# Performance work log

Hardware: AMD Instinct MI355X
Metric: run time of the kernel (lower is better)

Reference implementation:

```python
import jax, jax.numpy as jnp
import numpy as np

DIM = 1024
SEQ_LEN = 4096
K = 256
HEADS = 16
DIM_HEAD = DIM // HEADS  # 64
BATCH = 4


def setup_inputs() -> dict:
    key = jax.random.key(0)
    ks = jax.random.split(key, 8)
    x = jax.random.normal(ks[0], (BATCH, SEQ_LEN, DIM), dtype=jnp.float32)
    # nn.Linear weights are [out, in]; y = x @ W.T
    std_lin = 1.0 / np.sqrt(DIM)
    Wq = jax.random.uniform(ks[1], (HEADS * DIM_HEAD, DIM), minval=-std_lin, maxval=std_lin, dtype=jnp.float32)
    Wk = jax.random.uniform(ks[2], (HEADS * DIM_HEAD, DIM), minval=-std_lin, maxval=std_lin, dtype=jnp.float32)
    Wv = jax.random.uniform(ks[3], (HEADS * DIM_HEAD, DIM), minval=-std_lin, maxval=std_lin, dtype=jnp.float32)
    # proj_k/proj_v init_: uniform(-1/sqrt(k), 1/sqrt(k)) on [seq_len, k]
    std_p = 1.0 / np.sqrt(K)
    proj_k = jax.random.uniform(ks[4], (SEQ_LEN, K), minval=-std_p, maxval=std_p, dtype=jnp.float32)
    proj_v = jax.random.uniform(ks[5], (SEQ_LEN, K), minval=-std_p, maxval=std_p, dtype=jnp.float32)
    std_o = 1.0 / np.sqrt(HEADS * DIM_HEAD)
    Wo = jax.random.uniform(ks[6], (DIM, HEADS * DIM_HEAD), minval=-std_o, maxval=std_o, dtype=jnp.float32)
    bo = jax.random.uniform(ks[7], (DIM,), minval=-std_o, maxval=std_o, dtype=jnp.float32)
    return {"x": x, "Wq": Wq, "Wk": Wk, "Wv": Wv, "proj_k": proj_k, "proj_v": proj_v, "Wo": Wo, "bo": bo}


def reference(x, Wq, Wk, Wv, proj_k, proj_v, Wo, bo):
    b, n, d = x.shape
    h, dh, k = HEADS, DIM_HEAD, K
    # q/k/v projections
    q = jnp.einsum('bnd,ed->bne', x, Wq)            # [b, n, h*dh]
    keys = jnp.einsum('bnd,ed->bne', x, Wk)         # [b, n, h*dh]
    vals = jnp.einsum('bnd,ed->bne', x, Wv)         # [b, n, h*dh]
    # low-rank projection along sequence: [b, n, e] x [n, k] -> [b, k, e]
    keys = jnp.einsum('bne,nk->bke', keys, proj_k[:n])
    vals = jnp.einsum('bne,nk->bke', vals, proj_v[:n])
    # split heads
    q = q.reshape(b, n, h, dh).transpose(0, 2, 1, 3)        # [b, h, n, dh]
    keys = keys.reshape(b, k, h, dh).transpose(0, 2, 1, 3)  # [b, h, k, dh]
    vals = vals.reshape(b, k, h, dh).transpose(0, 2, 1, 3)  # [b, h, k, dh]
    dots = jnp.einsum('bhnd,bhkd->bhnk', q, keys) * (dh ** -0.5)
    attn = jax.nn.softmax(dots, axis=-1)
    out = jnp.einsum('bhnk,bhkd->bhnd', attn, vals)
    out = out.transpose(0, 2, 1, 3).reshape(b, n, h * dh)
    return jnp.einsum('bne,oe->bno', out, Wo) + bo
```

## Files before the change

### kernel.cpp

```cpp
#include <hip/hip_runtime.h>
#include <hip/hip_bf16.h>
#include <stdint.h>

typedef unsigned short u16;
typedef __attribute__((ext_vector_type(8))) short bf16x8;
typedef __attribute__((ext_vector_type(4))) float f32x4;

#define DEV __device__ __forceinline__

DEV u16 f2bf(float f) {
  union { float f; unsigned u; } v; v.f = f;
  unsigned r = (v.u + 0x7fffu + ((v.u >> 16) & 1u)) >> 16;
  return (u16)r;
}

DEV unsigned pk2(float lo, float hi) {
  union { __hip_bfloat162 h; unsigned u; } c;
  c.h = __float22bfloat162_rn(make_float2(lo, hi));
  return c.u;
}

DEV f32x4 mfma16(bf16x8 a, bf16x8 b, f32x4 c) {
  return __builtin_amdgcn_mfma_f32_16x16x32_bf16(a, b, c, 0, 0, 0);
}

DEV void gload_lds16(const u16* g, u16* l) {
  __builtin_amdgcn_global_load_lds((const __attribute__((address_space(1))) void*)g,
                                   (__attribute__((address_space(3))) void*)l, 16, 0, 0);
}

#define QSCALE 0.18033688011112042f

__global__ void cvt_xpose_kernel(const float* __restrict__ src, u16* __restrict__ dst_rm,
                                 u16* __restrict__ dst_tp, int R, int C,
                                 long zS, long zRM, long zTP) {
  __shared__ u16 tile[64][72];
  src += (size_t)blockIdx.z * zS;
  dst_tp += (size_t)blockIdx.z * zTP;
  int r0 = blockIdx.y * 64, c0 = blockIdx.x * 64;
  int tr = threadIdx.x >> 2, tc = (threadIdx.x & 3) * 16;
  const float* s = src + (size_t)(r0 + tr) * C + c0 + tc;
  u16 loc[16];
#pragma unroll
  for (int q = 0; q < 4; ++q) {
    float4 v = ((const float4*)s)[q];
    loc[q * 4 + 0] = f2bf(v.x); loc[q * 4 + 1] = f2bf(v.y);
    loc[q * 4 + 2] = f2bf(v.z); loc[q * 4 + 3] = f2bf(v.w);
  }
#pragma unroll
  for (int i = 0; i < 16; ++i) tile[tr][tc + i] = loc[i];
  if (dst_rm) {
    u16* d = dst_rm + (size_t)blockIdx.z * zRM + (size_t)(r0 + tr) * C + c0 + tc;
    *(bf16x8*)d = *(const bf16x8*)&loc[0];
    *(bf16x8*)(d + 8) = *(const bf16x8*)&loc[8];
  }
  __syncthreads();
  u16 tmp[16];
#pragma unroll
  for (int i = 0; i < 16; ++i) tmp[i] = tile[tc + i][tr];
  u16* d = dst_tp + (size_t)(c0 + tr) * R + r0 + tc;
  *(bf16x8*)d = *(const bf16x8*)&tmp[0];
  *(bf16x8*)(d + 8) = *(const bf16x8*)&tmp[8];
}

__global__ void cvt_w4_kernel(const float* __restrict__ s0, const float* __restrict__ s1,
                              const float* __restrict__ s2, const float* __restrict__ s3,
                              u16* __restrict__ d0, u16* __restrict__ d1,
                              u16* __restrict__ d2, u16* __restrict__ d3) {
  const float* s; u16* d;
  switch (blockIdx.y) {
    case 0: s = s0; d = d0; break;
    case 1: s = s1; d = d1; break;
    case 2: s = s2; d = d2; break;
    default: s = s3; d = d3; break;
  }
  int i = blockIdx.x * 256 + threadIdx.x;
  float4 v = ((const float4*)s)[i];
  ushort4 o; o.x = f2bf(v.x); o.y = f2bf(v.y); o.z = f2bf(v.z); o.w = f2bf(v.w);
  ((ushort4*)d)[i] = o;
}

__global__ void reduce4_kernel(const float* __restrict__ part, u16* __restrict__ out) {
  int i = blockIdx.x * 256 + threadIdx.x;
  const float4* p = (const float4*)part;
  float4 a = p[i], b = p[i + 524288], c = p[i + 1048576], d = p[i + 1572864];
  ushort4 o;
  o.x = f2bf(a.x + b.x + c.x + d.x);
  o.y = f2bf(a.y + b.y + c.y + d.y);
  o.z = f2bf(a.z + b.z + c.z + d.z);
  o.w = f2bf(a.w + b.w + c.w + d.w);
  ((ushort4*)out)[i] = o;
}

template<int OMODE>
__global__ __launch_bounds__(256, 4)
void gemm_bt_kernel(const u16* __restrict__ A, const u16* __restrict__ Bt,
                    const u16* __restrict__ Bt2, void* __restrict__ Cout,
                    u16* __restrict__ CoutT, const float* __restrict__ bias, float cscale,
                    int ldA, int ldB, int ldC, int Klen,
                    long zA, long zB, long zC, int bMod, long kChunkA, long kChunkB) {
  __shared__ __align__(16) u16 smA[2][128 * 32];
  __shared__ __align__(16) u16 smB[2][128 * 32];
  const int t = threadIdx.x;
  const int lane = t & 63, wave = t >> 6;
  const int wm = wave & 1, wn = wave >> 1;
  const int g = lane >> 4, r = lane & 15;
  const int id = blockIdx.y * gridDim.x + blockIdx.x;
  const int cpx = (gridDim.x * gridDim.y) >> 3;
  const int s = (id & 7) * cpx + (id >> 3);
  const int bx = s % gridDim.x, by = s / gridDim.x;
  const int z = blockIdx.z;
  const int b = z % bMod, kc = z / bMod;
  const u16* Ab = A + (size_t)b * zA + (size_t)kc * kChunkA;
  const u16* Bbase = (Bt2 && (b & 1)) ? Bt2 : Bt;
  const u16* Bb = Bbase + (size_t)b * zB + (size_t)kc * kChunkB;
  const int m0 = by * 128, n0 = bx * 128;
  const int srow = t >> 2;
  const int lslot = ((t & 3) + 4 - ((srow >> 1) & 3)) & 3;

  f32x4 acc[4][4];
#pragma unroll
  for (int m = 0; m < 4; ++m)
#pragma unroll
    for (int n = 0; n < 4; ++n) acc[m][n] = f32x4{0.f, 0.f, 0.f, 0.f};

  auto STAGE = [&](int buf, int k0) {
#pragma unroll
    for (int p = 0; p < 2; ++p) {
      int row = p * 64 + srow;
      gload_lds16(Ab + (size_t)(m0 + row) * ldA + k0 + lslot * 8, &smA[buf][p * 2048 + wave * 512]);
      gload_lds16(Bb + (size_t)(n0 + row) * ldB + k0 + lslot * 8, &smB[buf][p * 2048 + wave * 512]);
    }
  };

  const int nt = Klen >> 5;
  STAGE(0, 0);
  __syncthreads();
  int cur = 0;
  for (int it = 0; it < nt; ++it) {
    if (it + 1 < nt) STAGE(cur ^ 1, (it + 1) << 5);
    bf16x8 af[4], bfr[4];
#pragma unroll
    for (int m = 0; m < 4; ++m) {
      int row = wm * 64 + m * 16 + r;
      int ps = (g + (row >> 1)) & 3;
      af[m] = *(const bf16x8*)&smA[cur][row * 32 + ps * 8];
    }
#pragma unroll
    for (int n = 0; n < 4; ++n) {
      int row = wn * 64 + n * 16 + r;
      int ps = (g + (row >> 1)) & 3;
      bfr[n] = *(const bf16x8*)&smB[cur][row * 32 + ps * 8];
    }
#pragma unroll
    for (int m = 0; m < 4; ++m)
#pragma unroll
      for (int n = 0; n < 4; ++n)
        acc[m][n] = mfma16(af[m], bfr[n], acc[m][n]);
    __syncthreads();
    cur ^= 1;
  }

  if constexpr (OMODE == 0) {
    u16* C = (u16*)Cout + (size_t)z * zC;
#pragma unroll
    for (int n = 0; n < 4; ++n) {
      int col = n0 + wn * 64 + n * 16 + r;
#pragma unroll
      for (int m = 0; m < 4; ++m) {
        int rowb = m0 + wm * 64 + m * 16 + 4 * g;
#pragma unroll
        for (int rr = 0; rr < 4; ++rr)
          C[(size_t)(rowb + rr) * ldC + col] = f2bf(acc[m][n][rr] * cscale);
      }
    }
  } else if constexpr (OMODE == 2) {
    float* myF = ((float*)(wave < 2 ? (void*)&smA[0][0] : (void*)&smB[0][0])) + (wave & 1) * 2048;
    float* Cg = (float*)Cout + (size_t)z * zC + (size_t)(m0 + wm * 64) * ldC + n0 + wn * 64;
#pragma unroll
    for (int np = 0; np < 2; ++np) {
#pragma unroll
      for (int n2 = 0; n2 < 2; ++n2)
#pragma unroll
        for (int m = 0; m < 4; ++m)
#pragma unroll
          for (int rr = 0; rr < 4; ++rr) {
            int rl = m * 16 + 4 * g + rr;
            int cl = n2 * 16 + r;
            myF[rl * 32 + ((((cl >> 2) ^ (rl & 7)) & 7) << 2) + (cl & 3)] =
                acc[m][np * 2 + n2][rr];
          }
      __syncthreads();
#pragma unroll
      for (int i = 0; i < 8; ++i) {
        int idx = i * 64 + lane;
        int row = idx >> 3, c = idx & 7;
        float4 v = *(const float4*)&myF[row * 32 + (((c ^ (row & 7)) & 7) << 2)];
        *(float4*)&Cg[(size_t)row * ldC + np * 32 + c * 4] = v;
      }
      __syncthreads();
    }
  } else if constexpr (OMODE == 3) {
    if ((z & 1) == 0) {
      u16* C = (u16*)Cout + (size_t)(z >> 1) * zC;
#pragma unroll
      for (int n = 0; n < 4; ++n) {
        int col = n0 + wn * 64 + n * 16 + r;
#pragma unroll
        for (int m = 0; m < 4; ++m) {
          int rowb = m0 + wm * 64 + m * 16 + 4 * g;
#pragma unroll
          for (int rr = 0; rr < 4; ++rr)
            C[(size_t)(rowb + rr) * ldC + col] = f2bf(acc[m][n][rr]);
        }
      }
    } else {
      u16* C = CoutT + (size_t)(z >> 1) * zC;
#pragma unroll
      for (int n = 0; n < 4; ++n) {
        int col = n0 + wn * 64 + n * 16 + r;
#pragma unroll
        for (int m = 0; m < 4; ++m) {
          int rowb = m0 + wm * 64 + m * 16 + 4 * g;
          ushort4 o;
          o.x = f2bf(acc[m][n][0]); o.y = f2bf(acc[m][n][1]);
          o.z = f2bf(acc[m][n][2]); o.w = f2bf(acc[m][n][3]);
          *(ushort4*)&C[(size_t)col * 256 + rowb] = o;
        }
      }
    }
  } else {
    float* C = (float*)Cout + (size_t)z * zC;
#pragma unroll
    for (int n = 0; n < 4; ++n) {
      int col = n0 + wn * 64 + n * 16 + r;
      float bv = (OMODE == 1) ? bias[col] : 0.f;
#pragma unroll
      for (int m = 0; m < 4; ++m) {
        int rowb = m0 + wm * 64 + m * 16 + 4 * g;
#pragma unroll
        for (int rr = 0; rr < 4; ++rr)
          C[(size_t)(rowb + rr) * ldC + col] = acc[m][n][rr] + bv;
      }
    }
  }
}

__global__ __launch_bounds__(512, 4)
void qgemm128_kernel(const u16* __restrict__ A, const u16* __restrict__ Bt,
                     u16* __restrict__ Cout, float cscale,
                     int ldA, int ldB, int ldC, int Klen) {
  __shared__ __align__(16) u16 lds[24576];
  const int t = threadIdx.x;
  const int lane = t & 63, wave = t >> 6;
  const int g = lane >> 4, r = lane & 15;
  const int wm = wave >> 2, wn = wave & 3;
  const int id = blockIdx.y * gridDim.x + blockIdx.x;
  const int cpx = (gridDim.x * gridDim.y) >> 3;
  const int s = (id & 7) * cpx + (id >> 3);
  const int bx = s & 3, by = s >> 2;
  const int m0 = by * 128, n0 = bx * 256;

  const int srow = t >> 2;
  const int lslot = ((t & 3) + 4 - ((srow >> 1) & 3)) & 3;

  auto STAGE = [&](int buf, int k0) {
    gload_lds16(A + (size_t)(m0 + srow) * ldA + k0 + lslot * 8,
                lds + buf * 4096 + t * 8);
#pragma unroll
    for (int p = 0; p < 2; ++p)
      gload_lds16(Bt + (size_t)(n0 + p * 128 + srow) * ldB + k0 + lslot * 8,
                  lds + 8192 + buf * 8192 + p * 4096 + t * 8);
  };

  f32x4 acc[4][4];
#pragma unroll
  for (int m = 0; m < 4; ++m)
#pragma unroll
    for (int n = 0; n < 4; ++n) acc[m][n] = f32x4{0.f, 0.f, 0.f, 0.f};

  const int nt = Klen >> 5;
  STAGE(0, 0);
  __syncthreads();
  int cur = 0;
  for (int it = 0; it < nt; ++it) {
    if (it + 1 < nt) STAGE(cur ^ 1, (it + 1) << 5);
    const u16* Ab = lds + cur * 4096;
    const u16* Bb = lds + 8192 + cur * 8192;
    bf16x8 af[4], bfr[4];
#pragma unroll
    for (int m = 0; m < 4; ++m) {
      int row = wm * 64 + m * 16 + r;
      int ps = (g + (row >> 1)) & 3;
      af[m] = *(const bf16x8*)&Ab[row * 32 + ps * 8];
    }
#pragma unroll
    for (int n = 0; n < 4; ++n) {
      int row = wn * 64 + n * 16 + r;
      int ps = (g + (row >> 1)) & 3;
      bfr[n] = *(const bf16x8*)&Bb[row * 32 + ps * 8];
    }
    __builtin_amdgcn_s_setprio(1);
#pragma unroll
    for (int m = 0; m < 4; ++m)
#pragma unroll
      for (int n = 0; n < 4; ++n)
        acc[m][n] = mfma16(af[m], bfr[n], acc[m][n]);
    __builtin_amdgcn_s_setprio(0);
    __syncthreads();
    cur ^= 1;
  }

  u16* myT = lds + wave * 2048;
  u16* Cg = Cout + (size_t)(m0 + wm * 64) * ldC + n0 + wn * 64;
#pragma unroll
  for (int np = 0; np < 2; ++np) {
#pragma unroll
    for (int n2 = 0; n2 < 2; ++n2)
#pragma unroll
      for (int m = 0; m < 4; ++m)
#pragma unroll
        for (int rr = 0; rr < 4; ++rr) {
          int rl = m * 16 + 4 * g + rr;
          int cl = n2 * 16 + r;
          myT[rl * 32 + (((cl >> 3) ^ (rl & 3)) << 3) + (cl & 7)] =
              f2bf(acc[m][np * 2 + n2][rr] * cscale);
        }
#pragma unroll
    for (int i = 0; i < 4; ++i) {
      int idx = i * 64 + lane;
      int row = idx >> 2, c = idx & 3;
      bf16x8 v = *(const bf16x8*)&myT[row * 32 + ((c ^ (row & 3)) << 3)];
      *(bf16x8*)&Cg[(size_t)row * ldC + np * 32 + c * 8] = v;
    }
  }
}

#define MFMA_CLUSTER(MH, NH, AF, BV)                                                    \
  do {                                                                                  \
    __builtin_amdgcn_s_setprio(1);                                                      \
    _Pragma("unroll")                                                                   \
    for (int mi = 0; mi < 4; ++mi)                                                      \
      _Pragma("unroll")                                                                 \
      for (int ni = 0; ni < 2; ++ni) {                                                  \
        acc[(MH)*4+mi][(NH)*2+ni] = mfma16(AF[mi][0], BV[ni][0], acc[(MH)*4+mi][(NH)*2+ni]); \
        acc[(MH)*4+mi][(NH)*2+ni] = mfma16(AF[mi][1], BV[ni][1], acc[(MH)*4+mi][(NH)*2+ni]); \
      }                                                                                 \
    __builtin_amdgcn_s_setprio(0);                                                      \
  } while (0)

#define ENDBAR(W)                                                                       \
  do {                                                                                  \
    if ((W) == 1) asm volatile("s_waitcnt vmcnt(4)" ::: "memory");                      \
    if ((W) == 2) asm volatile("s_waitcnt vmcnt(0)" ::: "memory");                      \
    __builtin_amdgcn_s_barrier();                                                       \
  } while (0)

template<int OMODE>
__global__ __launch_bounds__(512, 1)
void gemm256_kernel(const u16* __restrict__ A, const u16* __restrict__ Bt,
                    void* __restrict__ Cout, const float* __restrict__ bias,
                    float cscale, int ldA, int ldB, int ldC, int Klen) {
  __shared__ __align__(16) u16 lds[65536];
  const int t = threadIdx.x;
  const int lane = t & 63, wave = t >> 6;
  const int g = lane >> 4, r = lane & 15, rm = r & 7;
  const int wm = wave >> 2, wn = wave & 3;
  const int id = blockIdx.y * 4 + blockIdx.x;
  const int sw = (id & 7) * 32 + (id >> 3);
  const int bx = sw & 3, by = sw >> 2;
  const int m0 = by * 256, n0 = bx * 256;

  const int trow = t >> 3, tslot = t & 7;
  const int sslot = tslot ^ (trow & 7);
  const u16* Asrc = A + (size_t)(m0 + trow) * ldA + sslot * 8;
  const u16* Bsrc = Bt + sslot * 8;
  const int bRow0 = n0 + (trow >> 5) * 64 + (trow & 31);
  const int bRow1 = n0 + (2 + (trow >> 5)) * 64 + (trow & 31);

  u16* const A0 = lds;
  u16* const A1 = lds + 16384;
  u16* const B0 = lds + 32768;
  u16* const B1 = lds + 49152;

  auto stageA = [&](u16* buf, int h, int k0) {
    u16* d = buf + h * 8192 + t * 8;
    const u16* s0 = Asrc + (size_t)(h * 64) * ldA + k0;
    gload_lds16(s0, d);
    gload_lds16(s0 + (size_t)128 * ldA, d + 4096);
  };
  auto stageB = [&](u16* buf, int h, int k0) {
    u16* d = buf + h * 8192 + t * 8;
    gload_lds16(Bsrc + (size_t)(bRow0 + h * 32) * ldB + k0, d);
    gload_lds16(Bsrc + (size_t)(bRow1 + h * 32) * ldB + k0, d + 4096);
  };

  const int aoff = wm * 64 + r;
  const int boff = wn * 32 + r;

  auto loadA = [&](bf16x8 af[4][2], const u16* base, int MH) {
#pragma unroll
    for (int mi = 0; mi < 4; ++mi) {
      const u16* rp = base + (MH * 128 + aoff + mi * 16) * 64;
      af[mi][0] = *(const bf16x8*)&rp[(g ^ rm) * 8];
      af[mi][1] = *(const bf16x8*)&rp[((4 + g) ^ rm) * 8];
    }
  };
  auto loadB = [&](bf16x8 bv[2][2], const u16* base, int NH) {
#pragma unroll
    for (int ni = 0; ni < 2; ++ni) {
      const u16* rp = base + (NH * 128 + boff + ni * 16) * 64;
      bv[ni][0] = *(const bf16x8*)&rp[(g ^ rm) * 8];
      bv[ni][1] = *(const bf16x8*)&rp[((4 + g) ^ rm) * 8];
    }
  };

  f32x4 acc[8][4];
#pragma unroll
  for (int m = 0; m < 8; ++m)
#pragma unroll
    for (int n = 0; n < 4; ++n) acc[m][n] = f32x4{0.f, 0.f, 0.f, 0.f};

  stageA(A0, 0, 0); stageB(B0, 0, 0); stageA(A0, 1, 0); stageB(B0, 1, 0);
  stageA(A1, 0, 64); stageB(B1, 0, 64);
  asm volatile("s_waitcnt vmcnt(4)" ::: "memory");
  __builtin_amdgcn_s_barrier();

  const int nt = Klen >> 6;
  for (int j = 0; j < (nt >> 1); ++j) {
    const int ta = 2 * j, tb = ta + 1;
    const int more = (ta + 2 < nt);
    const int kb = tb * 64, kn = (ta + 2) * 64, kn2 = (tb + 2) * 64;
    bf16x8 af[4][2], bv0[2][2], bv1[2][2];
    loadA(af, A0, 0); loadB(bv0, B0, 0);
    stageA(A1, 1, kb);
    MFMA_CLUSTER(0, 0, af, bv0); ENDBAR(0);
    loadB(bv1, B0, 1);
    stageB(B1, 1, kb);
    MFMA_CLUSTER(0, 1, af, bv1); ENDBAR(0);
    loadA(af, A0, 1);
    if (more) stageA(A0, 0, kn);
    MFMA_CLUSTER(1, 0, af, bv0); ENDBAR(0);
    if (more) stageB(B0, 0, kn);
    MFMA_CLUSTER(1, 1, af, bv1); ENDBAR(more ? 1 : 2);
    loadA(af, A1, 0); loadB(bv0, B1, 0);
    if (more) stageA(A0, 1, kn);
    MFMA_CLUSTER(0, 0, af, bv0); ENDBAR(0);
    loadB(bv1, B1, 1);
    if (more) stageB(B0, 1, kn);
    MFMA_CLUSTER(0, 1, af, bv1); ENDBAR(0);
    loadA(af, A1, 1);
    if (more) stageA(A1, 0, kn2);
    MFMA_CLUSTER(1, 0, af, bv0); ENDBAR(0);
    if (more) stageB(B1, 0, kn2);
    MFMA_CLUSTER(1, 1, af, bv1); ENDBAR(more ? 1 : 2);
  }

  if constexpr (OMODE == 0) {
    u16* myT = lds + wave * 8192;
#pragma unroll
    for (int m = 0; m < 8; ++m)
#pragma unroll
      for (int n = 0; n < 4; ++n)
#pragma unroll
        for (int rr = 0; rr < 4; ++rr) {
          int rl = m * 16 + 4 * g + rr;
          int cl = n * 16 + r;
          myT[rl * 64 + (((cl >> 3) ^ (rl & 7)) << 3) + (cl & 7)] = f2bf(acc[m][n][rr] * cscale);
        }
    u16* Cg = (u16*)Cout + (size_t)(m0 + wm * 128) * ldC + n0 + wn * 64;
#pragma unroll
    for (int i = 0; i < 16; ++i) {
      int idx = i * 64 + lane;
      int row = idx >> 3, c8 = idx & 7;
      bf16x8 v = *(const bf16x8*)&myT[row * 64 + ((c8 ^ (row & 7)) << 3)];
      *(bf16x8*)&Cg[(size_t)row * ldC + c8 * 8] = v;
    }
  } else {
    float* myF = (float*)lds + wave * 4096;
    float bvn[4];
#pragma unroll
    for (int n = 0; n < 4; ++n) bvn[n] = bias[n0 + wn * 64 + n * 16 + r];
    float* Cg = (float*)Cout + (size_t)(m0 + wm * 128) * ldC + n0 + wn * 64;
#pragma unroll
    for (int half = 0; half < 2; ++half) {
#pragma unroll
      for (int m2 = 0; m2 < 4; ++m2)
#pragma unroll
        for (int n = 0; n < 4; ++n)
#pragma unroll
          for (int rr = 0; rr < 4; ++rr) {
            int rl = m2 * 16 + 4 * g + rr;
            int cl = n * 16 + r;
            myF[rl * 64 + (((cl >> 2) ^ (rl & 15)) << 2) + (cl & 3)] =
                acc[half * 4 + m2][n][rr] + bvn[n];
          }
#pragma unroll
      for (int i = 0; i < 16; ++i) {
        int idx = i * 64 + lane;
        int row = idx >> 4, c4 = idx & 15;
        float4 v = *(const float4*)&myF[row * 64 + ((c4 ^ (row & 15)) << 2)];
        *(float4*)&Cg[(size_t)(half * 64 + row) * ldC + c4 * 4] = v;
      }
    }
  }
}

__global__ __launch_bounds__(256, 3)
void attn_kernel(const u16* __restrict__ Q, const u16* __restrict__ Kl,
                 const u16* __restrict__ VT, u16* __restrict__ Out) {
  __shared__ __align__(16) u16 sm[24576];
  const int t = threadIdx.x, lane = t & 63, w = t >> 6;
  const int g = lane >> 4, r = lane & 15;
  const int id = (blockIdx.y << 6) | blockIdx.x;
  const int s = (id & 7) * (gridDim.y << 3) + (id >> 3);
  const int b = blockIdx.z, h = s >> 6, n0 = (s & 63) * 64;
  const u16* Kb = Kl + (size_t)b * 262144 + h * 64;
  const u16* Vb = VT + (size_t)b * 262144 + (size_t)(h * 64) * 256;
  u16* vbase = sm + 16384;

  const int vd = t >> 2;
  const int vsl = (t & 3) ^ (vd & 3);
  auto stage_slice = [&](int kk) {
    gload_lds16(Vb + (size_t)vd * 256 + kk * 32 + vsl * 8,
                vbase + (kk & 3) * 2048 + w * 512);
  };

#pragma unroll
  for (int p = 0; p < 8; ++p) {
    int row = p * 32 + (t >> 3);
    int ls = ((t & 7) + 8 - (row & 7)) & 7;
    gload_lds16(Kb + (size_t)row * 1024 + ls * 8, sm + p * 2048 + w * 512);
  }
#pragma unroll
  for (int kk = 0; kk < 4; ++kk) stage_slice(kk);
  const int qrow = n0 + w * 16 + r;
  const u16* Qp = Q + ((size_t)(b * 4096 + qrow)) * 1024 + h * 64 + g * 8;
  bf16x8 aq0 = *(const bf16x8*)Qp;
  bf16x8 aq1 = *(const bf16x8*)(Qp + 32);
  asm volatile("s_waitcnt vmcnt(4)" ::: "memory");
  __builtin_amdgcn_s_barrier();

  f32x4 dotv[16];
  __builtin_amdgcn_s_setprio(1);
#pragma unroll
  for (int kf = 0; kf < 16; ++kf) {
    int row = kf * 16 + r;
    bf16x8 kb0 = *(const bf16x8*)&sm[row * 64 + ((g + row) & 7) * 8];
    bf16x8 kb1 = *(const bf16x8*)&sm[row * 64 + ((4 + g + row) & 7) * 8];
    f32x4 d = f32x4{0.f, 0.f, 0.f, 0.f};
    d = mfma16(kb0, aq0, d);
    d = mfma16(kb1, aq1, d);
    dotv[kf] = d;
  }
  __builtin_amdgcn_s_setprio(0);
  asm volatile("s_waitcnt vmcnt(3)" ::: "memory");
  __builtin_amdgcn_s_barrier();

  float mx = -3.4e38f;
#pragma unroll
  for (int kf = 0; kf < 16; ++kf)
    mx = fmaxf(mx, fmaxf(fmaxf(dotv[kf][0], dotv[kf][1]), fmaxf(dotv[kf][2], dotv[kf][3])));
  mx = fmaxf(mx, __shfl_xor(mx, 16, 64));
  mx = fmaxf(mx, __shfl_xor(mx, 32, 64));
  float ssum = 0.f;
#pragma unroll
  for (int kf = 0; kf < 16; ++kf)
#pragma unroll
    for (int j = 0; j < 4; ++j) {
      float p = __builtin_amdgcn_exp2f(dotv[kf][j] - mx);
      dotv[kf][j] = p;
      ssum += p;
    }
  ssum += __shfl_xor(ssum, 16, 64);
  ssum += __shfl_xor(ssum, 32, 64);
  const float inv = 1.f / ssum;
  float invv[4];
#pragma unroll
  for (int rr = 0; rr < 4; ++rr) invv[rr] = __shfl(inv, 4 * g + rr, 64);

  const int q16 = w * 16 + r;
  const int qx = (q16 & 7) << 3;
#pragma unroll
  for (int kf = 0; kf < 16; ++kf) {
    uint2 val;
    val.x = pk2(dotv[kf][0], dotv[kf][1]);
    val.y = pk2(dotv[kf][2], dotv[kf][3]);
    *(uint2*)&sm[(q16 * 256 + kf * 16 + 4 * g) ^ qx] = val;
  }

  f32x4 oacc[4];
#pragma unroll
  for (int df = 0; df < 4; ++df) oacc[df] = f32x4{0.f, 0.f, 0.f, 0.f};
#pragma unroll
  for (int kk = 0; kk < 8; ++kk) {
    bf16x8 ap = *(const bf16x8*)&sm[(q16 * 256 + kk * 32 + g * 8) ^ qx];
    const u16* vb = vbase + (kk & 3) * 2048;
    __builtin_amdgcn_s_setprio(1);
#pragma unroll
    for (int df = 0; df < 4; ++df) {
      int d = df * 16 + r;
      bf16x8 bv = *(const bf16x8*)&vb[d * 32 + (g ^ (d & 3)) * 8];
      oacc[df] = mfma16(ap, bv, oacc[df]);
    }
    __builtin_amdgcn_s_setprio(0);
    if (kk < 7) {
      if (kk < 5)       asm volatile("s_waitcnt vmcnt(2)" ::: "memory");
      else if (kk == 5) asm volatile("s_waitcnt vmcnt(1)" ::: "memory");
      else              asm volatile("s_waitcnt vmcnt(0)" ::: "memory");
      __builtin_amdgcn_s_barrier();
      if (kk < 4) stage_slice(kk + 4);
    }
  }

  u16* myO = sm + w * 4096;
#pragma unroll
  for (int df = 0; df < 4; ++df)
#pragma unroll
    for (int rr = 0; rr < 4; ++rr) {
      int row = 4 * g + rr;
      int col = df * 16 + r;
      myO[row * 64 + (((col >> 3) ^ (row & 7)) << 3) + (col & 7)] = f2bf(oacc[df][rr] * invv[rr]);
    }
#pragma unroll
  for (int i = 0; i < 2; ++i) {
    int idx = i * 64 + lane;
    int row = idx >> 3, c8 = idx & 7;
    bf16x8 v = *(const bf16x8*)&myO[row * 64 + ((c8 ^ (row & 7)) << 3)];
    *(bf16x8*)&Out[((size_t)(b * 4096 + n0 + w * 16 + row)) * 1024 + h * 64 + c8 * 8] = v;
  }
}

extern "C" void kernel_launch(void* const* d_in, const int* in_sizes, int n_in,
                              void* d_out, int out_size, void* d_ws, size_t ws_size,
                              hipStream_t stream) {
  const float* x  = (const float*)d_in[0];
  const float* Wq = (const float*)d_in[1];
  const float* Wk = (const float*)d_in[2];
  const float* Wv = (const float*)d_in[3];
  const float* pk = (const float*)d_in[4];
  const float* pv = (const float*)d_in[5];
  const float* Wo = (const float*)d_in[6];
  const float* bo = (const float*)d_in[7];

  u16* ws = (u16*)d_ws;
  u16* xbf   = ws;
  u16* xT    = xbf + 16777216;
  u16* wqb   = xT + 16777216;
  u16* wkb   = wqb + 1048576;
  u16* wvb   = wkb + 1048576;
  u16* wob   = wvb + 1048576;
  u16* projT = wob + 1048576;
  u16* Qb    = projT + 2097152;
  u16* xp    = Qb + 16777216;
  u16* klow  = xp + 2097152;
  u16* vT    = klow + 1048576;
  u16* aout  = xbf;
  float* xp_part = (float*)Qb;

  cvt_xpose_kernel<<<dim3(16, 64, 4), 256, 0, stream>>>(x, xbf, xT, 4096, 1024,
                                                        4194304, 4194304, 4194304);
  cvt_w4_kernel<<<dim3(1024, 4), 256, 0, stream>>>(Wq, Wk, Wv, Wo, wqb, wkb, wvb, wob);
  cvt_xpose_kernel<<<dim3(4, 64, 1), 256, 0, stream>>>(pk, nullptr, projT, 4096, 256, 0, 0, 0);
  cvt_xpose_kernel<<<dim3(4, 64, 1), 256, 0, stream>>>(pv, nullptr, projT + 1048576, 4096, 256, 0, 0, 0);
  gemm_bt_kernel<2><<<dim3(32, 4, 4), 256, 0, stream>>>(
      projT, xT, nullptr, (void*)xp_part, nullptr, nullptr, 1.f,
      4096, 4096, 4096, 1024, 0, 0, 2097152, 1, 1024, 1024);
  reduce4_kernel<<<2048, 256, 0, stream>>>(xp_part, xp);
  gemm_bt_kernel<3><<<dim3(8, 2, 8), 256, 0, stream>>>(
      xp, wkb, wvb, (void*)klow, vT, nullptr, 1.f,
      4096, 1024, 1024, 1024, 1048576, 0, 262144, 2, 1024, 0);
  qgemm128_kernel<<<dim3(4, 128), 512, 0, stream>>>(
      xbf, wqb, Qb, QSCALE, 1024, 1024, 1024, 1024);
  attn_kernel<<<dim3(64, 16, 4), 256, 0, stream>>>(Qb, klow, vT, aout);
  gemm256_kernel<1><<<dim3(4, 64), 512, 0, stream>>>(
      aout, wob, d_out, bo, 1.f, 1024, 1024, 1024, 1024);
}
```

Measured before the change: 213.2 us.

## Triple-buffer qgemm128 prefetch and reuse it for output projection

The 128x256 Q-projection GEMM moves from double to triple-buffered LDS staging. It prefetches two K-steps ahead and uses explicit vmcnt waits plus a single barrier per iteration instead of two __syncthreads. The kernel is templated with an fp32+bias epilogue, so the final output projection now runs on it instead of the large 256x256 gemm256 kernel with occupancy 1. This trades a hand-scheduled, larger-tile kernel for smaller tiles with higher occupancy and deeper prefetch, at the cost of more LDS per block.

```diff
diff --git a/kernel.cpp b/kernel.cpp
--- a/kernel.cpp
+++ b/kernel.cpp
@@ -246,11 +246,12 @@
   }
 }
 
+template<int OMODE>
 __global__ __launch_bounds__(512, 4)
 void qgemm128_kernel(const u16* __restrict__ A, const u16* __restrict__ Bt,
-                     u16* __restrict__ Cout, float cscale,
-                     int ldA, int ldB, int ldC, int Klen) {
-  __shared__ __align__(16) u16 lds[24576];
+                     void* __restrict__ Cout, const float* __restrict__ bias,
+                     float cscale, int ldA, int ldB, int ldC, int Klen) {
+  __shared__ __align__(16) u16 lds[36864];
   const int t = threadIdx.x;
   const int lane = t & 63, wave = t >> 6;
   const int g = lane >> 4, r = lane & 15;
@@ -270,7 +271,7 @@
 #pragma unroll
     for (int p = 0; p < 2; ++p)
       gload_lds16(Bt + (size_t)(n0 + p * 128 + srow) * ldB + k0 + lslot * 8,
-                  lds + 8192 + buf * 8192 + p * 4096 + t * 8);
+                  lds + 12288 + buf * 8192 + p * 4096 + t * 8);
   };
 
   f32x4 acc[4][4];
@@ -281,12 +282,16 @@
 
   const int nt = Klen >> 5;
   STAGE(0, 0);
-  __syncthreads();
+  STAGE(1, 32);
+  asm volatile("s_waitcnt vmcnt(3)" ::: "memory");
+  __builtin_amdgcn_s_barrier();
+
   int cur = 0;
   for (int it = 0; it < nt; ++it) {
-    if (it + 1 < nt) STAGE(cur ^ 1, (it + 1) << 5);
+    int pre = cur + 2; if (pre >= 3) pre -= 3;
+    if (it + 2 < nt) STAGE(pre, (it + 2) << 5);
     const u16* Ab = lds + cur * 4096;
-    const u16* Bb = lds + 8192 + cur * 8192;
+    const u16* Bb = lds + 12288 + cur * 8192;
     bf16x8 af[4], bfr[4];
 #pragma unroll
     for (int m = 0; m < 4; ++m) {
@@ -307,200 +312,64 @@
       for (int n = 0; n < 4; ++n)
         acc[m][n] = mfma16(af[m], bfr[n], acc[m][n]);
     __builtin_amdgcn_s_setprio(0);
-    __syncthreads();
-    cur ^= 1;
-  }
-
-  u16* myT = lds + wave * 2048;
-  u16* Cg = Cout + (size_t)(m0 + wm * 64) * ldC + n0 + wn * 64;
-#pragma unroll
-  for (int np = 0; np < 2; ++np) {
-#pragma unroll
-    for (int n2 = 0; n2 < 2; ++n2)
-#pragma unroll
-      for (int m = 0; m < 4; ++m)
-#pragma unroll
-        for (int rr = 0; rr < 4; ++rr) {
-          int rl = m * 16 + 4 * g + rr;
-          int cl = n2 * 16 + r;
-          myT[rl * 32 + (((cl >> 3) ^ (rl & 3)) << 3) + (cl & 7)] =
-              f2bf(acc[m][np * 2 + n2][rr] * cscale);
-        }
-#pragma unroll
-    for (int i = 0; i < 4; ++i) {
-      int idx = i * 64 + lane;
-      int row = idx >> 2, c = idx & 3;
-      bf16x8 v = *(const bf16x8*)&myT[row * 32 + ((c ^ (row & 3)) << 3)];
-      *(bf16x8*)&Cg[(size_t)row * ldC + np * 32 + c * 8] = v;
-    }
-  }
-}
-
-#define MFMA_CLUSTER(MH, NH, AF, BV)                                                    \
-  do {                                                                                  \
-    __builtin_amdgcn_s_setprio(1);                                                      \
-    _Pragma("unroll")                                                                   \
-    for (int mi = 0; mi < 4; ++mi)                                                      \
-      _Pragma("unroll")                                                                 \
-      for (int ni = 0; ni < 2; ++ni) {                                                  \
-        acc[(MH)*4+mi][(NH)*2+ni] = mfma16(AF[mi][0], BV[ni][0], acc[(MH)*4+mi][(NH)*2+ni]); \
-        acc[(MH)*4+mi][(NH)*2+ni] = mfma16(AF[mi][1], BV[ni][1], acc[(MH)*4+mi][(NH)*2+ni]); \
-      }                                                                                 \
-    __builtin_amdgcn_s_setprio(0);                                                      \
-  } while (0)
-
-#define ENDBAR(W)                                                                       \
-  do {                                                                                  \
-    if ((W) == 1) asm volatile("s_waitcnt vmcnt(4)" ::: "memory");                      \
-    if ((W) == 2) asm volatile("s_waitcnt vmcnt(0)" ::: "memory");                      \
-    __builtin_amdgcn_s_barrier();                                                       \
-  } while (0)
-
-template<int OMODE>
-__global__ __launch_bounds__(512, 1)
-void gemm256_kernel(const u16* __restrict__ A, const u16* __restrict__ Bt,
-                    void* __restrict__ Cout, const float* __restrict__ bias,
-                    float cscale, int ldA, int ldB, int ldC, int Klen) {
-  __shared__ __align__(16) u16 lds[65536];
-  const int t = threadIdx.x;
-  const int lane = t & 63, wave = t >> 6;
-  const int g = lane >> 4, r = lane & 15, rm = r & 7;
-  const int wm = wave >> 2, wn = wave & 3;
-  const int id = blockIdx.y * 4 + blockIdx.x;
-  const int sw = (id & 7) * 32 + (id >> 3);
-  const int bx = sw & 3, by = sw >> 2;
-  const int m0 = by * 256, n0 = bx * 256;
-
-  const int trow = t >> 3, tslot = t & 7;
-  const int sslot = tslot ^ (trow & 7);
-  const u16* Asrc = A + (size_t)(m0 + trow) * ldA + sslot * 8;
-  const u16* Bsrc = Bt + sslot * 8;
-  const int bRow0 = n0 + (trow >> 5) * 64 + (trow & 31);
-  const int bRow1 = n0 + (2 + (trow >> 5)) * 64 + (trow & 31);
-
-  u16* const A0 = lds;
-  u16* const A1 = lds + 16384;
-  u16* const B0 = lds + 32768;
-  u16* const B1 = lds + 49152;
-
-  auto stageA = [&](u16* buf, int h, int k0) {
-    u16* d = buf + h * 8192 + t * 8;
-    const u16* s0 = Asrc + (size_t)(h * 64) * ldA + k0;
-    gload_lds16(s0, d);
-    gload_lds16(s0 + (size_t)128 * ldA, d + 4096);
-  };
-  auto stageB = [&](u16* buf, int h, int k0) {
-    u16* d = buf + h * 8192 + t * 8;
-    gload_lds16(Bsrc + (size_t)(bRow0 + h * 32) * ldB + k0, d);
-    gload_lds16(Bsrc + (size_t)(bRow1 + h * 32) * ldB + k0, d + 4096);
-  };
-
-  const int aoff = wm * 64 + r;
-  const int boff = wn * 32 + r;
-
-  auto loadA = [&](bf16x8 af[4][2], const u16* base, int MH) {
-#pragma unroll
-    for (int mi = 0; mi < 4; ++mi) {
-      const u16* rp = base + (MH * 128 + aoff + mi * 16) * 64;
-      af[mi][0] = *(const bf16x8*)&rp[(g ^ rm) * 8];
-      af[mi][1] = *(const bf16x8*)&rp[((4 + g) ^ rm) * 8];
-    }
-  };
-  auto loadB = [&](bf16x8 bv[2][2], const u16* base, int NH) {
-#pragma unroll
-    for (int ni = 0; ni < 2; ++ni) {
-      const u16* rp = base + (NH * 128 + boff + ni * 16) * 64;
-      bv[ni][0] = *(const bf16x8*)&rp[(g ^ rm) * 8];
-      bv[ni][1] = *(const bf16x8*)&rp[((4 + g) ^ rm) * 8];
-    }
-  };
-
-  f32x4 acc[8][4];
-#pragma unroll
-  for (int m = 0; m < 8; ++m)
-#pragma unroll
-    for (int n = 0; n < 4; ++n) acc[m][n] = f32x4{0.f, 0.f, 0.f, 0.f};
-
-  stageA(A0, 0, 0); stageB(B0, 0, 0); stageA(A0, 1, 0); stageB(B0, 1, 0);
-  stageA(A1, 0, 64); stageB(B1, 0, 64);
-  asm volatile("s_waitcnt vmcnt(4)" ::: "memory");
+    if (it + 1 < nt) {
+      if (it + 2 < nt) asm volatile("s_waitcnt vmcnt(3)" ::: "memory");
+      else             asm volatile("s_waitcnt vmcnt(0)" ::: "memory");
+      __builtin_amdgcn_s_barrier();
+    }
+    cur = cur + 1; if (cur >= 3) cur -= 3;
+  }
   __builtin_amdgcn_s_barrier();
 
-  const int nt = Klen >> 6;
-  for (int j = 0; j < (nt >> 1); ++j) {
-    const int ta = 2 * j, tb = ta + 1;
-    const int more = (ta + 2 < nt);
-    const int kb = tb * 64, kn = (ta + 2) * 64, kn2 = (tb + 2) * 64;
-    bf16x8 af[4][2], bv0[2][2], bv1[2][2];
-    loadA(af, A0, 0); loadB(bv0, B0, 0);
-    stageA(A1, 1, kb);
-    MFMA_CLUSTER(0, 0, af, bv0); ENDBAR(0);
-    loadB(bv1, B0, 1);
-    stageB(B1, 1, kb);
-    MFMA_CLUSTER(0, 1, af, bv1); ENDBAR(0);
-    loadA(af, A0, 1);
-    if (more) stageA(A0, 0, kn);
-    MFMA_CLUSTER(1, 0, af, bv0); ENDBAR(0);
-    if (more) stageB(B0, 0, kn);
-    MFMA_CLUSTER(1, 1, af, bv1); ENDBAR(more ? 1 : 2);
-    loadA(af, A1, 0); loadB(bv0, B1, 0);
-    if (more) stageA(A0, 1, kn);
-    MFMA_CLUSTER(0, 0, af, bv0); ENDBAR(0);
-    loadB(bv1, B1, 1);
-    if (more) stageB(B0, 1, kn);
-    MFMA_CLUSTER(0, 1, af, bv1); ENDBAR(0);
-    loadA(af, A1, 1);
-    if (more) stageA(A1, 0, kn2);
-    MFMA_CLUSTER(1, 0, af, bv0); ENDBAR(0);
-    if (more) stageB(B1, 0, kn2);
-    MFMA_CLUSTER(1, 1, af, bv1); ENDBAR(more ? 1 : 2);
-  }
-
   if constexpr (OMODE == 0) {
-    u16* myT = lds + wave * 8192;
-#pragma unroll
-    for (int m = 0; m < 8; ++m)
-#pragma unroll
-      for (int n = 0; n < 4; ++n)
-#pragma unroll
-        for (int rr = 0; rr < 4; ++rr) {
-          int rl = m * 16 + 4 * g + rr;
-          int cl = n * 16 + r;
-          myT[rl * 64 + (((cl >> 3) ^ (rl & 7)) << 3) + (cl & 7)] = f2bf(acc[m][n][rr] * cscale);
-        }
-    u16* Cg = (u16*)Cout + (size_t)(m0 + wm * 128) * ldC + n0 + wn * 64;
-#pragma unroll
-    for (int i = 0; i < 16; ++i) {
-      int idx = i * 64 + lane;
-      int row = idx >> 3, c8 = idx & 7;
-      bf16x8 v = *(const bf16x8*)&myT[row * 64 + ((c8 ^ (row & 7)) << 3)];
-      *(bf16x8*)&Cg[(size_t)row * ldC + c8 * 8] = v;
+    u16* myT = lds + wave * 2048;
+    u16* Cg = (u16*)Cout + (size_t)(m0 + wm * 64) * ldC + n0 + wn * 64;
+#pragma unroll
+    for (int np = 0; np < 2; ++np) {
+#pragma unroll
+      for (int n2 = 0; n2 < 2; ++n2)
+#pragma unroll
+        for (int m = 0; m < 4; ++m)
+#pragma unroll
+          for (int rr = 0; rr < 4; ++rr) {
+            int rl = m * 16 + 4 * g + rr;
+            int cl = n2 * 16 + r;
+            myT[rl * 32 + (((cl >> 3) ^ (rl & 3)) << 3) + (cl & 7)] =
+                f2bf(acc[m][np * 2 + n2][rr] * cscale);
+          }
+#pragma unroll
+      for (int i = 0; i < 4; ++i) {
+        int idx = i * 64 + lane;
+        int row = idx >> 2, c = idx & 3;
+        bf16x8 v = *(const bf16x8*)&myT[row * 32 + ((c ^ (row & 3)) << 3)];
+        *(bf16x8*)&Cg[(size_t)row * ldC + np * 32 + c * 8] = v;
+      }
     }
   } else {
-    float* myF = (float*)lds + wave * 4096;
+    float* myF = (float*)lds + wave * 2048;
     float bvn[4];
 #pragma unroll
     for (int n = 0; n < 4; ++n) bvn[n] = bias[n0 + wn * 64 + n * 16 + r];
-    float* Cg = (float*)Cout + (size_t)(m0 + wm * 128) * ldC + n0 + wn * 64;
-#pragma unroll
-    for (int half = 0; half < 2; ++half) {
-#pragma unroll
-      for (int m2 = 0; m2 < 4; ++m2)
-#pragma unroll
-        for (int n = 0; n < 4; ++n)
+    float* Cg = (float*)Cout + (size_t)(m0 + wm * 64) * ldC + n0 + wn * 64;
+#pragma unroll
+    for (int np = 0; np < 2; ++np) {
+#pragma unroll
+      for (int n2 = 0; n2 < 2; ++n2)
+#pragma unroll
+        for (int m = 0; m < 4; ++m)
 #pragma unroll
           for (int rr = 0; rr < 4; ++rr) {
-            int rl = m2 * 16 + 4 * g + rr;
-            int cl = n * 16 + r;
-            myF[rl * 64 + (((cl >> 2) ^ (rl & 15)) << 2) + (cl & 3)] =
-                acc[half * 4 + m2][n][rr] + bvn[n];
+            int rl = m * 16 + 4 * g + rr;
+            int cl = n2 * 16 + r;
+            myF[rl * 32 + ((((cl >> 2) ^ (rl & 7)) & 7) << 2) + (cl & 3)] =
+                acc[m][np * 2 + n2][rr] + bvn[np * 2 + n2];
           }
 #pragma unroll
-      for (int i = 0; i < 16; ++i) {
+      for (int i = 0; i < 8; ++i) {
         int idx = i * 64 + lane;
-        int row = idx >> 4, c4 = idx & 15;
-        float4 v = *(const float4*)&myF[row * 64 + ((c4 ^ (row & 15)) << 2)];
-        *(float4*)&Cg[(size_t)(half * 64 + row) * ldC + c4 * 4] = v;
+        int row = idx >> 3, c = idx & 7;
+        float4 v = *(const float4*)&myF[row * 32 + (((c ^ (row & 7)) & 7) << 2)];
+        *(float4*)&Cg[(size_t)row * ldC + np * 32 + c * 4] = v;
       }
     }
   }
@@ -670,9 +539,9 @@
   gemm_bt_kernel<3><<<dim3(8, 2, 8), 256, 0, stream>>>(
       xp, wkb, wvb, (void*)klow, vT, nullptr, 1.f,
       4096, 1024, 1024, 1024, 1048576, 0, 262144, 2, 1024, 0);
-  qgemm128_kernel<<<dim3(4, 128), 512, 0, stream>>>(
-      xbf, wqb, Qb, QSCALE, 1024, 1024, 1024, 1024);
+  qgemm128_kernel<0><<<dim3(4, 128), 512, 0, stream>>>(
+      xbf, wqb, (void*)Qb, nullptr, QSCALE, 1024, 1024, 1024, 1024);
   attn_kernel<<<dim3(64, 16, 4), 256, 0, stream>>>(Qb, klow, vT, aout);
-  gemm256_kernel<1><<<dim3(4, 64), 512, 0, stream>>>(
+  qgemm128_kernel<1><<<dim3(4, 128), 512, 0, stream>>>(
       aout, wob, d_out, bo, 1.f, 1024, 1024, 1024, 1024);
 }
```

New measurement: 210.4 us. About the same (-1.3%).
